# Performance work log

Measured on AMD Instinct MI355X. Metric: run time of the kernel, lower is better.

## Reference

```python
import jax, jax.numpy as jnp
import numpy as np

N_ATOMS = 4096
N_NEIGH = 32
IN_F = 128
HID = 256
OUT_F = 128
N_SPECIES = 64


def setup_inputs() -> dict:
    key = jax.random.key(0)
    k1, k2, k3, k4, k5, k6 = jax.random.split(key, 6)
    # kaiming-uniform-ish init scales (exact init doesn't matter for correctness testing)
    s1 = 1.0 / np.sqrt(IN_F)
    s2 = 1.0 / np.sqrt(HID)
    return {
        "features": jax.random.normal(k1, (N_ATOMS, N_NEIGH, IN_F), dtype=jnp.float32),
        "species_idx": jax.random.randint(k2, (N_ATOMS,), 0, N_SPECIES, dtype=jnp.int64 if jax.config.jax_enable_x64 else jnp.int32),
        "W1": jax.random.uniform(k3, (N_SPECIES, HID, IN_F), jnp.float32, -s1, s1),
        "b1": jax.random.uniform(k4, (N_SPECIES, HID), jnp.float32, -s1, s1),
        "W2": jax.random.uniform(k5, (N_SPECIES, OUT_F, HID), jnp.float32, -s2, s2),
        "b2": jax.random.uniform(k6, (N_SPECIES, OUT_F), jnp.float32, -s2, s2),
    }


def reference(features, species_idx, W1, b1, W2, b2):
    # Per-atom species-conditioned 2-layer MLP with SiLU after the hidden layer.
    # features: (A, N, in); W[idx]: (A, out, in) gathered per atom (as in torch W[idx]).
    x = jnp.einsum("ani,ahi->anh", features, W1[species_idx]) + b1[species_idx][:, None, :]
    x = jax.nn.silu(x)
    x = jnp.einsum("anh,aoh->ano", x, W2[species_idx]) + b2[species_idx][:, None, :]
    return x  # (A, N, out)
```

## Files before the change

kernel.cpp:

```cpp
#include <hip/hip_runtime.h>

typedef __attribute__((ext_vector_type(8))) short short8;
typedef __attribute__((ext_vector_type(4))) float f32x4;

#define N_ATOMS 4096
#define N_NEIGH 32
#define IN_F 128
#define HID 256
#define OUT_F 128
#define N_SPECIES 64
#define GRP 8
#define MAX_GROUPS 576

struct HL { short h, l; };
__device__ __forceinline__ HL split2(float v) {
  unsigned u = __float_as_uint(v);
  float lo = v - __uint_as_float(u & 0xFFFF0000u);
  HL o;
  o.h = (short)(u >> 16);
  o.l = (short)(__float_as_uint(lo) >> 16);
  return o;
}

__global__ __launch_bounds__(256) void prep_kernel(
    const float* __restrict__ W1, const float* __restrict__ W2,
    const int* __restrict__ sp_idx,
    unsigned short* __restrict__ w1h, unsigned short* __restrict__ w1l,
    unsigned short* __restrict__ w2h, unsigned short* __restrict__ w2l,
    int* __restrict__ atom_order, int* __restrict__ grp_sp,
    int* __restrict__ grp_base, int* __restrict__ grp_cnt,
    int* __restrict__ n_groups) {
  const int t = threadIdx.x;
  if (blockIdx.x == 0) {
    __shared__ int cnt[N_SPECIES], off[N_SPECIES], cur[N_SPECIES], gb[N_SPECIES];
    if (t < N_SPECIES) cnt[t] = 0;
    __syncthreads();
    for (int a = t; a < N_ATOMS; a += 256) atomicAdd(&cnt[sp_idx[a]], 1);
    __syncthreads();
    if (t == 0) {
      int o = 0, g = 0;
      for (int s = 0; s < N_SPECIES; ++s) {
        off[s] = o; cur[s] = o; gb[s] = g;
        o += cnt[s];
        g += (cnt[s] + GRP - 1) / GRP;
      }
      *n_groups = g;
    }
    __syncthreads();
    for (int a = t; a < N_ATOMS; a += 256) {
      int s = sp_idx[a];
      atom_order[atomicAdd(&cur[s], 1)] = a;
    }
    if (t < N_SPECIES) {
      const int c = cnt[t], base = off[t], g0 = gb[t];
      const int ng = (c + GRP - 1) / GRP;
      for (int j = 0; j < ng; ++j) {
        grp_sp[g0 + j]   = t;
        grp_base[g0 + j] = base + j * GRP;
        grp_cnt[g0 + j]  = min(GRP, c - j * GRP);
      }
    }
    return;
  }
  const int NV = (N_SPECIES * HID * IN_F) / 4;
  const int nsplit = (gridDim.x - 1) * 256;
  for (int v = (blockIdx.x - 1) * 256 + t; v < 2 * NV; v += nsplit) {
    const float4* src; unsigned short* dh; unsigned short* dl; int j;
    if (v < NV) { src = (const float4*)W1; dh = w1h; dl = w1l; j = v; }
    else        { src = (const float4*)W2; dh = w2h; dl = w2l; j = v - NV; }
    float4 f = src[j];
    float vv[4] = {f.x, f.y, f.z, f.w};
    ushort4 h, l;
    HL s0 = split2(vv[0]); h.x = (unsigned short)s0.h; l.x = (unsigned short)s0.l;
    HL s1 = split2(vv[1]); h.y = (unsigned short)s1.h; l.y = (unsigned short)s1.l;
    HL s2 = split2(vv[2]); h.z = (unsigned short)s2.h; l.z = (unsigned short)s2.l;
    HL s3 = split2(vv[3]); h.w = (unsigned short)s3.h; l.w = (unsigned short)s3.l;
    ((ushort4*)dh)[j] = h;
    ((ushort4*)dl)[j] = l;
  }
}

__global__ __launch_bounds__(512, 2) void mlp_kernel(
    const float* __restrict__ feat,
    const float* __restrict__ b1g, const float* __restrict__ b2g,
    const unsigned short* __restrict__ w1h, const unsigned short* __restrict__ w1l,
    const unsigned short* __restrict__ w2h, const unsigned short* __restrict__ w2l,
    const int* __restrict__ atom_order, const int* __restrict__ grp_sp,
    const int* __restrict__ grp_base, const int* __restrict__ grp_cnt,
    const int* __restrict__ n_groups,
    float* __restrict__ out) {
  const int bid = blockIdx.x;
  const int g = (bid & 7) * (MAX_GROUPS / 8) + (bid >> 3);
  if (g >= *n_groups) return;
  const int s = grp_sp[g];
  const int abase = grp_base[g];
  const int cnt = grp_cnt[g];
  const int tid = threadIdx.x;
  const int wave = tid >> 6, lane = tid & 63;
  const int q = lane >> 4, r = lane & 15;

  __shared__ short lw1[2][2][32 * IN_F];
  __shared__ short lw2[2][2][OUT_F * 32];
  __shared__ float lx[8][N_NEIGH * 32];

  const bool active = (wave < cnt);
  int atom = 0;

  const int plane = wave >> 1, half = wave & 1;
  const bool isw1 = (plane < 2);
  const unsigned short* pl = (plane == 0) ? w1h : (plane == 1) ? w1l
                           : (plane == 2) ? w2h : w2l;
  const char* gplane = (const char*)pl + (long)s * (HID * IN_F) * 2;
  const int hcstride = isw1 ? (32 * IN_F * 2) : (32 * 2);
  int srcoff[4], dstoff[4];
#pragma unroll
  for (int it = 0; it < 4; ++it) {
    const int b = half * 4096 + it * 1024 + lane * 16;
    if (isw1) {
      const int row = b >> 8;
      srcoff[it] = row * (IN_F * 2) + ((b & 255) ^ ((row & 7) << 4));
    } else {
      const int o = b >> 6;
      srcoff[it] = o * (HID * 2) + ((b & 63) ^ (((o >> 1) & 3) << 4));
    }
    dstoff[it] = b;
  }
  char* lplane0 = isw1 ? (char*)lw1[0][plane] : (char*)lw2[0][plane - 2];

  auto STAGE = [&](int buf, int hc) {
    const char* base = gplane + hc * hcstride;
    char* lp = lplane0 + buf * 16384;
#pragma unroll
    for (int it = 0; it < 4; ++it) {
      __builtin_amdgcn_global_load_lds(
          (const __attribute__((address_space(1))) unsigned int*)(base + srcoff[it]),
          (__attribute__((address_space(3))) unsigned int*)(lp + dstoff[it]),
          16, 0, 0);
    }
  };

  STAGE(0, 0);

  short8 fh[2][4], fl[2][4];
  if (active) {
    atom = atom_order[abase + wave];
    const float* fb = feat + (long)atom * (N_NEIGH * IN_F);
#pragma unroll
    for (int nt = 0; nt < 2; ++nt)
#pragma unroll
      for (int ks = 0; ks < 4; ++ks) {
        const float* p = fb + (16 * nt + r) * IN_F + 32 * ks + 8 * q;
        float4 v0 = *(const float4*)p;
        float4 v1 = *(const float4*)(p + 4);
        float vv[8] = {v0.x, v0.y, v0.z, v0.w, v1.x, v1.y, v1.z, v1.w};
        short8 h8, l8;
#pragma unroll
        for (int j = 0; j < 8; ++j) {
          HL hl = split2(vv[j]);
          h8[j] = hl.h;
          l8[j] = hl.l;
        }
        fh[nt][ks] = h8;
        fl[nt][ks] = l8;
      }
  }

  float b2v[8];
#pragma unroll
  for (int ot = 0; ot < 8; ++ot) b2v[ot] = b2g[s * OUT_F + 16 * ot + r];

  f32x4 oacc[2][8] = {};
  char* lxw = (char*)lx[wave];
  const int swz1 = (r & 7) << 4;
  const int swz2 = ((r >> 1) & 3) << 4;

  asm volatile("s_waitcnt vmcnt(0)" ::: "memory");
  __syncthreads();

  for (int hc = 0; hc < 8; ++hc) {
    const int buf = hc & 1;
    if (hc < 7) STAGE(buf ^ 1, hc + 1);

    if (active) {
      f32x4 xacc[2][2] = {};
      const char* L1h = (const char*)lw1[buf][0];
      const char* L1l = (const char*)lw1[buf][1];
#pragma unroll
      for (int ks = 0; ks < 4; ++ks) {
        const int koff = 64 * ks + 16 * q;
#pragma unroll
        for (int ht = 0; ht < 2; ++ht) {
          const int byte = (16 * ht + r) * 256 + (koff ^ swz1);
          short8 bh = *(const short8*)(L1h + byte);
          short8 bl = *(const short8*)(L1l + byte);
#pragma unroll
          for (int nt = 0; nt < 2; ++nt) {
            xacc[nt][ht] = __builtin_amdgcn_mfma_f32_16x16x32_bf16(fh[nt][ks], bh, xacc[nt][ht], 0, 0, 0);
            xacc[nt][ht] = __builtin_amdgcn_mfma_f32_16x16x32_bf16(fh[nt][ks], bl, xacc[nt][ht], 0, 0, 0);
            xacc[nt][ht] = __builtin_amdgcn_mfma_f32_16x16x32_bf16(fl[nt][ks], bh, xacc[nt][ht], 0, 0, 0);
          }
        }
      }
#pragma unroll
      for (int ht = 0; ht < 2; ++ht) {
        const float b1v = b1g[s * HID + hc * 32 + 16 * ht + r];
#pragma unroll
        for (int nt = 0; nt < 2; ++nt)
#pragma unroll
          for (int i = 0; i < 4; ++i) {
            const int n = 16 * nt + 4 * q + i;
            float v = xacc[nt][ht][i] + b1v;
            v = v * __builtin_amdgcn_rcpf(1.0f + __expf(-v));
            int byte = (n << 7) + ((r + 16 * ht) << 2);
            byte ^= (n & 7) << 4;
            *(float*)(lxw + byte) = v;
          }
      }
      short8 ah[2], al[2];
#pragma unroll
      for (int nt = 0; nt < 2; ++nt) {
        const int n = 16 * nt + r;
        const int base_b = (n << 7) + (q << 5);
        const int swz = (n & 7) << 4;
        float4 v0 = *(const float4*)(lxw + (base_b ^ swz));
        float4 v1 = *(const float4*)(lxw + ((base_b + 16) ^ swz));
        float vv[8] = {v0.x, v0.y, v0.z, v0.w, v1.x, v1.y, v1.z, v1.w};
        short8 h8, l8;
#pragma unroll
        for (int j = 0; j < 8; ++j) {
          HL hl = split2(vv[j]);
          h8[j] = hl.h;
          l8[j] = hl.l;
        }
        ah[nt] = h8;
        al[nt] = l8;
      }
      const char* L2h = (const char*)lw2[buf][0];
      const char* L2l = (const char*)lw2[buf][1];
#pragma unroll
      for (int ot = 0; ot < 8; ++ot) {
        const int byte = (16 * ot + r) * 64 + ((16 * q) ^ swz2);
        short8 bh = *(const short8*)(L2h + byte);
        short8 bl = *(const short8*)(L2l + byte);
#pragma unroll
        for (int nt = 0; nt < 2; ++nt) {
          oacc[nt][ot] = __builtin_amdgcn_mfma_f32_16x16x32_bf16(ah[nt], bh, oacc[nt][ot], 0, 0, 0);
          oacc[nt][ot] = __builtin_amdgcn_mfma_f32_16x16x32_bf16(ah[nt], bl, oacc[nt][ot], 0, 0, 0);
          oacc[nt][ot] = __builtin_amdgcn_mfma_f32_16x16x32_bf16(al[nt], bh, oacc[nt][ot], 0, 0, 0);
        }
      }
    }
    asm volatile("s_waitcnt vmcnt(0)" ::: "memory");
    __syncthreads();
  }

  if (active) {
    float* ob = out + (long)atom * (N_NEIGH * OUT_F);
#pragma unroll
    for (int nt = 0; nt < 2; ++nt)
#pragma unroll
      for (int ot = 0; ot < 8; ++ot)
#pragma unroll
        for (int i = 0; i < 4; ++i) {
          ob[(16 * nt + 4 * q + i) * OUT_F + 16 * ot + r] = oacc[nt][ot][i] + b2v[ot];
        }
  }
}

extern "C" void kernel_launch(void* const* d_in, const int* in_sizes, int n_in,
                              void* d_out, int out_size, void* d_ws, size_t ws_size,
                              hipStream_t stream) {
  const float* feat = (const float*)d_in[0];
  const int* sp     = (const int*)d_in[1];
  const float* W1   = (const float*)d_in[2];
  const float* b1   = (const float*)d_in[3];
  const float* W2   = (const float*)d_in[4];
  const float* b2   = (const float*)d_in[5];
  float* out = (float*)d_out;

  char* ws = (char*)d_ws;
  unsigned short* w1h = (unsigned short*)(ws + 0);
  unsigned short* w1l = (unsigned short*)(ws + 4194304);
  unsigned short* w2h = (unsigned short*)(ws + 8388608);
  unsigned short* w2l = (unsigned short*)(ws + 12582912);
  int* atom_order = (int*)(ws + 16777216);
  int* grp_sp     = (int*)(ws + 16777216 + 16384);
  int* grp_base   = (int*)(ws + 16777216 + 16384 + 4352);
  int* grp_cnt    = (int*)(ws + 16777216 + 16384 + 8704);
  int* n_groups   = (int*)(ws + 16777216 + 16384 + 13056);

  hipLaunchKernelGGL(prep_kernel, dim3(1025), dim3(256), 0, stream,
                     W1, W2, sp, w1h, w1l, w2h, w2l,
                     atom_order, grp_sp, grp_base, grp_cnt, n_groups);
  hipLaunchKernelGGL(mlp_kernel, dim3(MAX_GROUPS), dim3(512), 0, stream,
                     feat, b1, b2, w1h, w1l, w2h, w2l,
                     atom_order, grp_sp, grp_base, grp_cnt, n_groups, out);
}
```

Measured before the change: 205.7 us.

## Use single rounded bf16 weights and stage full species weights in LDS once

```diff
diff --git a/kernel.cpp b/kernel.cpp
--- a/kernel.cpp
+++ b/kernel.cpp
@@ -12,6 +12,11 @@
 #define GRP 8
 #define MAX_GROUPS 576
 
+__device__ __forceinline__ unsigned short f2bf(float f) {
+  unsigned u = __float_as_uint(f);
+  u += 0x7FFF + ((u >> 16) & 1);
+  return (unsigned short)(u >> 16);
+}
 struct HL { short h, l; };
 __device__ __forceinline__ HL split2(float v) {
   unsigned u = __float_as_uint(v);
@@ -25,8 +30,7 @@
 __global__ __launch_bounds__(256) void prep_kernel(
     const float* __restrict__ W1, const float* __restrict__ W2,
     const int* __restrict__ sp_idx,
-    unsigned short* __restrict__ w1h, unsigned short* __restrict__ w1l,
-    unsigned short* __restrict__ w2h, unsigned short* __restrict__ w2l,
+    unsigned short* __restrict__ w1h, unsigned short* __restrict__ w2h,
     int* __restrict__ atom_order, int* __restrict__ grp_sp,
     int* __restrict__ grp_base, int* __restrict__ grp_cnt,
     int* __restrict__ n_groups) {
@@ -65,30 +69,28 @@
   const int NV = (N_SPECIES * HID * IN_F) / 4;
   const int nsplit = (gridDim.x - 1) * 256;
   for (int v = (blockIdx.x - 1) * 256 + t; v < 2 * NV; v += nsplit) {
-    const float4* src; unsigned short* dh; unsigned short* dl; int j;
-    if (v < NV) { src = (const float4*)W1; dh = w1h; dl = w1l; j = v; }
-    else        { src = (const float4*)W2; dh = w2h; dl = w2l; j = v - NV; }
+    const float4* src; unsigned short* dh; int j;
+    if (v < NV) { src = (const float4*)W1; dh = w1h; j = v; }
+    else        { src = (const float4*)W2; dh = w2h; j = v - NV; }
     float4 f = src[j];
-    float vv[4] = {f.x, f.y, f.z, f.w};
-    ushort4 h, l;
-    HL s0 = split2(vv[0]); h.x = (unsigned short)s0.h; l.x = (unsigned short)s0.l;
-    HL s1 = split2(vv[1]); h.y = (unsigned short)s1.h; l.y = (unsigned short)s1.l;
-    HL s2 = split2(vv[2]); h.z = (unsigned short)s2.h; l.z = (unsigned short)s2.l;
-    HL s3 = split2(vv[3]); h.w = (unsigned short)s3.h; l.w = (unsigned short)s3.l;
+    ushort4 h;
+    h.x = f2bf(f.x); h.y = f2bf(f.y); h.z = f2bf(f.z); h.w = f2bf(f.w);
     ((ushort4*)dh)[j] = h;
-    ((ushort4*)dl)[j] = l;
   }
 }
 
 __global__ __launch_bounds__(512, 2) void mlp_kernel(
     const float* __restrict__ feat,
     const float* __restrict__ b1g, const float* __restrict__ b2g,
-    const unsigned short* __restrict__ w1h, const unsigned short* __restrict__ w1l,
-    const unsigned short* __restrict__ w2h, const unsigned short* __restrict__ w2l,
+    const unsigned short* __restrict__ w1h, const unsigned short* __restrict__ w2h,
     const int* __restrict__ atom_order, const int* __restrict__ grp_sp,
     const int* __restrict__ grp_base, const int* __restrict__ grp_cnt,
     const int* __restrict__ n_groups,
     float* __restrict__ out) {
+  extern __shared__ char smem[];
+  char* LW1 = smem;
+  char* LW2 = smem + 65536;
+
   const int bid = blockIdx.x;
   const int g = (bid & 7) * (MAX_GROUPS / 8) + (bid >> 3);
   if (g >= *n_groups) return;
@@ -98,50 +100,33 @@
   const int tid = threadIdx.x;
   const int wave = tid >> 6, lane = tid & 63;
   const int q = lane >> 4, r = lane & 15;
-
-  __shared__ short lw1[2][2][32 * IN_F];
-  __shared__ short lw2[2][2][OUT_F * 32];
-  __shared__ float lx[8][N_NEIGH * 32];
-
   const bool active = (wave < cnt);
+
+  {
+    const char* gw1 = (const char*)w1h + (long)s * (HID * IN_F * 2);
+    const char* gw2 = (const char*)w2h + (long)s * (OUT_F * HID * 2);
+#pragma unroll
+    for (int it = 0; it < 8; ++it) {
+      const int d = it * 8192 + tid * 16;
+      const int h = d >> 8, w = d & 255;
+      const int src = h * (IN_F * 2) + (w ^ ((h & 7) << 4));
+      __builtin_amdgcn_global_load_lds(
+          (const __attribute__((address_space(1))) unsigned int*)(gw1 + src),
+          (__attribute__((address_space(3))) unsigned int*)(LW1 + d), 16, 0, 0);
+    }
+#pragma unroll
+    for (int it = 0; it < 8; ++it) {
+      const int d = it * 8192 + tid * 16;
+      const int o = d >> 9, w = d & 511;
+      const int src = o * (HID * 2) + (w ^ ((o & 7) << 4));
+      __builtin_amdgcn_global_load_lds(
+          (const __attribute__((address_space(1))) unsigned int*)(gw2 + src),
+          (__attribute__((address_space(3))) unsigned int*)(LW2 + d), 16, 0, 0);
+    }
+  }
+
+  short8 fh[2][4], fl[2][4];
   int atom = 0;
-
-  const int plane = wave >> 1, half = wave & 1;
-  const bool isw1 = (plane < 2);
-  const unsigned short* pl = (plane == 0) ? w1h : (plane == 1) ? w1l
-                           : (plane == 2) ? w2h : w2l;
-  const char* gplane = (const char*)pl + (long)s * (HID * IN_F) * 2;
-  const int hcstride = isw1 ? (32 * IN_F * 2) : (32 * 2);
-  int srcoff[4], dstoff[4];
-#pragma unroll
-  for (int it = 0; it < 4; ++it) {
-    const int b = half * 4096 + it * 1024 + lane * 16;
-    if (isw1) {
-      const int row = b >> 8;
-      srcoff[it] = row * (IN_F * 2) + ((b & 255) ^ ((row & 7) << 4));
-    } else {
-      const int o = b >> 6;
-      srcoff[it] = o * (HID * 2) + ((b & 63) ^ (((o >> 1) & 3) << 4));
-    }
-    dstoff[it] = b;
-  }
-  char* lplane0 = isw1 ? (char*)lw1[0][plane] : (char*)lw2[0][plane - 2];
-
-  auto STAGE = [&](int buf, int hc) {
-    const char* base = gplane + hc * hcstride;
-    char* lp = lplane0 + buf * 16384;
-#pragma unroll
-    for (int it = 0; it < 4; ++it) {
-      __builtin_amdgcn_global_load_lds(
-          (const __attribute__((address_space(1))) unsigned int*)(base + srcoff[it]),
-          (__attribute__((address_space(3))) unsigned int*)(lp + dstoff[it]),
-          16, 0, 0);
-    }
-  };
-
-  STAGE(0, 0);
-
-  short8 fh[2][4], fl[2][4];
   if (active) {
     atom = atom_order[abase + wave];
     const float* fb = feat + (long)atom * (N_NEIGH * IN_F);
@@ -165,105 +150,85 @@
       }
   }
 
-  float b2v[8];
-#pragma unroll
-  for (int ot = 0; ot < 8; ++ot) b2v[ot] = b2g[s * OUT_F + 16 * ot + r];
-
-  f32x4 oacc[2][8] = {};
-  char* lxw = (char*)lx[wave];
-  const int swz1 = (r & 7) << 4;
-  const int swz2 = ((r >> 1) & 3) << 4;
-
   asm volatile("s_waitcnt vmcnt(0)" ::: "memory");
   __syncthreads();
 
+  if (!active) return;
+
+  f32x4 oacc[2][8] = {};
+  char* lxw = smem + 131072 + wave * 4096;
+  const int swz = (r & 7) << 4;
+  const float* b1s = b1g + s * HID;
+
   for (int hc = 0; hc < 8; ++hc) {
-    const int buf = hc & 1;
-    if (hc < 7) STAGE(buf ^ 1, hc + 1);
-
-    if (active) {
-      f32x4 xacc[2][2] = {};
-      const char* L1h = (const char*)lw1[buf][0];
-      const char* L1l = (const char*)lw1[buf][1];
-#pragma unroll
-      for (int ks = 0; ks < 4; ++ks) {
-        const int koff = 64 * ks + 16 * q;
-#pragma unroll
-        for (int ht = 0; ht < 2; ++ht) {
-          const int byte = (16 * ht + r) * 256 + (koff ^ swz1);
-          short8 bh = *(const short8*)(L1h + byte);
-          short8 bl = *(const short8*)(L1l + byte);
-#pragma unroll
-          for (int nt = 0; nt < 2; ++nt) {
-            xacc[nt][ht] = __builtin_amdgcn_mfma_f32_16x16x32_bf16(fh[nt][ks], bh, xacc[nt][ht], 0, 0, 0);
-            xacc[nt][ht] = __builtin_amdgcn_mfma_f32_16x16x32_bf16(fh[nt][ks], bl, xacc[nt][ht], 0, 0, 0);
-            xacc[nt][ht] = __builtin_amdgcn_mfma_f32_16x16x32_bf16(fl[nt][ks], bh, xacc[nt][ht], 0, 0, 0);
-          }
+    f32x4 xacc[2][2] = {};
+#pragma unroll
+    for (int ks = 0; ks < 4; ++ks) {
+      const int ib = ((32 * ks + 8 * q) * 2) ^ swz;
+#pragma unroll
+      for (int ht = 0; ht < 2; ++ht) {
+        const int row = 32 * hc + 16 * ht + r;
+        short8 bh = *(const short8*)(LW1 + row * 256 + ib);
+        xacc[0][ht] = __builtin_amdgcn_mfma_f32_16x16x32_bf16(fh[0][ks], bh, xacc[0][ht], 0, 0, 0);
+        xacc[1][ht] = __builtin_amdgcn_mfma_f32_16x16x32_bf16(fh[1][ks], bh, xacc[1][ht], 0, 0, 0);
+        xacc[0][ht] = __builtin_amdgcn_mfma_f32_16x16x32_bf16(fl[0][ks], bh, xacc[0][ht], 0, 0, 0);
+        xacc[1][ht] = __builtin_amdgcn_mfma_f32_16x16x32_bf16(fl[1][ks], bh, xacc[1][ht], 0, 0, 0);
+      }
+    }
+#pragma unroll
+    for (int ht = 0; ht < 2; ++ht) {
+      const float b1v = b1s[hc * 32 + 16 * ht + r];
+#pragma unroll
+      for (int nt = 0; nt < 2; ++nt)
+#pragma unroll
+        for (int i = 0; i < 4; ++i) {
+          const int n = 16 * nt + 4 * q + i;
+          float v = xacc[nt][ht][i] + b1v;
+          v = v * __builtin_amdgcn_rcpf(1.0f + __expf(-v));
+          const int byte = n * 128 + (((16 * ht + r) * 4) ^ ((q & 1) << 6));
+          *(float*)(lxw + byte) = v;
         }
-      }
-#pragma unroll
-      for (int ht = 0; ht < 2; ++ht) {
-        const float b1v = b1g[s * HID + hc * 32 + 16 * ht + r];
-#pragma unroll
-        for (int nt = 0; nt < 2; ++nt)
-#pragma unroll
-          for (int i = 0; i < 4; ++i) {
-            const int n = 16 * nt + 4 * q + i;
-            float v = xacc[nt][ht][i] + b1v;
-            v = v * __builtin_amdgcn_rcpf(1.0f + __expf(-v));
-            int byte = (n << 7) + ((r + 16 * ht) << 2);
-            byte ^= (n & 7) << 4;
-            *(float*)(lxw + byte) = v;
-          }
-      }
-      short8 ah[2], al[2];
-#pragma unroll
-      for (int nt = 0; nt < 2; ++nt) {
-        const int n = 16 * nt + r;
-        const int base_b = (n << 7) + (q << 5);
-        const int swz = (n & 7) << 4;
-        float4 v0 = *(const float4*)(lxw + (base_b ^ swz));
-        float4 v1 = *(const float4*)(lxw + ((base_b + 16) ^ swz));
-        float vv[8] = {v0.x, v0.y, v0.z, v0.w, v1.x, v1.y, v1.z, v1.w};
-        short8 h8, l8;
-#pragma unroll
-        for (int j = 0; j < 8; ++j) {
-          HL hl = split2(vv[j]);
-          h8[j] = hl.h;
-          l8[j] = hl.l;
-        }
-        ah[nt] = h8;
-        al[nt] = l8;
-      }
-      const char* L2h = (const char*)lw2[buf][0];
-      const char* L2l = (const char*)lw2[buf][1];
-#pragma unroll
-      for (int ot = 0; ot < 8; ++ot) {
-        const int byte = (16 * ot + r) * 64 + ((16 * q) ^ swz2);
-        short8 bh = *(const short8*)(L2h + byte);
-        short8 bl = *(const short8*)(L2l + byte);
-#pragma unroll
-        for (int nt = 0; nt < 2; ++nt) {
-          oacc[nt][ot] = __builtin_amdgcn_mfma_f32_16x16x32_bf16(ah[nt], bh, oacc[nt][ot], 0, 0, 0);
-          oacc[nt][ot] = __builtin_amdgcn_mfma_f32_16x16x32_bf16(ah[nt], bl, oacc[nt][ot], 0, 0, 0);
-          oacc[nt][ot] = __builtin_amdgcn_mfma_f32_16x16x32_bf16(al[nt], bh, oacc[nt][ot], 0, 0, 0);
-        }
-      }
-    }
-    asm volatile("s_waitcnt vmcnt(0)" ::: "memory");
-    __syncthreads();
-  }
-
-  if (active) {
-    float* ob = out + (long)atom * (N_NEIGH * OUT_F);
+    }
+    short8 ah[2], al[2];
+#pragma unroll
+    for (int nt = 0; nt < 2; ++nt) {
+      const int n = 16 * nt + r;
+      const int base_b = n * 128 + ((32 * q) ^ (((r >> 2) & 1) << 6));
+      float4 v0 = *(const float4*)(lxw + base_b);
+      float4 v1 = *(const float4*)(lxw + base_b + 16);
+      float vv[8] = {v0.x, v0.y, v0.z, v0.w, v1.x, v1.y, v1.z, v1.w};
+      short8 h8, l8;
+#pragma unroll
+      for (int j = 0; j < 8; ++j) {
+        HL hl = split2(vv[j]);
+        h8[j] = hl.h;
+        l8[j] = hl.l;
+      }
+      ah[nt] = h8;
+      al[nt] = l8;
+    }
+    const int kb = ((32 * hc + 8 * q) * 2) ^ swz;
+#pragma unroll
+    for (int ot = 0; ot < 8; ++ot) {
+      const int row = 16 * ot + r;
+      short8 bw = *(const short8*)(LW2 + row * 512 + kb);
+      oacc[0][ot] = __builtin_amdgcn_mfma_f32_16x16x32_bf16(ah[0], bw, oacc[0][ot], 0, 0, 0);
+      oacc[1][ot] = __builtin_amdgcn_mfma_f32_16x16x32_bf16(ah[1], bw, oacc[1][ot], 0, 0, 0);
+      oacc[0][ot] = __builtin_amdgcn_mfma_f32_16x16x32_bf16(al[0], bw, oacc[0][ot], 0, 0, 0);
+      oacc[1][ot] = __builtin_amdgcn_mfma_f32_16x16x32_bf16(al[1], bw, oacc[1][ot], 0, 0, 0);
+    }
+  }
+
+  float* ob = out + (long)atom * (N_NEIGH * OUT_F);
+#pragma unroll
+  for (int ot = 0; ot < 8; ++ot) {
+    const float b2v = b2g[s * OUT_F + 16 * ot + r];
 #pragma unroll
     for (int nt = 0; nt < 2; ++nt)
 #pragma unroll
-      for (int ot = 0; ot < 8; ++ot)
-#pragma unroll
-        for (int i = 0; i < 4; ++i) {
-          ob[(16 * nt + 4 * q + i) * OUT_F + 16 * ot + r] = oacc[nt][ot][i] + b2v[ot];
-        }
+      for (int i = 0; i < 4; ++i) {
+        ob[(16 * nt + 4 * q + i) * OUT_F + 16 * ot + r] = oacc[nt][ot][i] + b2v;
+      }
   }
 }
 
@@ -280,19 +245,20 @@
 
   char* ws = (char*)d_ws;
   unsigned short* w1h = (unsigned short*)(ws + 0);
-  unsigned short* w1l = (unsigned short*)(ws + 4194304);
-  unsigned short* w2h = (unsigned short*)(ws + 8388608);
-  unsigned short* w2l = (unsigned short*)(ws + 12582912);
-  int* atom_order = (int*)(ws + 16777216);
-  int* grp_sp     = (int*)(ws + 16777216 + 16384);
-  int* grp_base   = (int*)(ws + 16777216 + 16384 + 4352);
-  int* grp_cnt    = (int*)(ws + 16777216 + 16384 + 8704);
-  int* n_groups   = (int*)(ws + 16777216 + 16384 + 13056);
+  unsigned short* w2h = (unsigned short*)(ws + 4194304);
+  int* atom_order = (int*)(ws + 8388608);
+  int* grp_sp     = (int*)(ws + 8388608 + 16384);
+  int* grp_base   = (int*)(ws + 8388608 + 16384 + 4352);
+  int* grp_cnt    = (int*)(ws + 8388608 + 16384 + 8704);
+  int* n_groups   = (int*)(ws + 8388608 + 16384 + 13056);
+
+  hipFuncSetAttribute((const void*)mlp_kernel,
+                      hipFuncAttributeMaxDynamicSharedMemorySize, 163840);
 
   hipLaunchKernelGGL(prep_kernel, dim3(1025), dim3(256), 0, stream,
-                     W1, W2, sp, w1h, w1l, w2h, w2l,
+                     W1, W2, sp, w1h, w2h,
                      atom_order, grp_sp, grp_base, grp_cnt, n_groups);
-  hipLaunchKernelGGL(mlp_kernel, dim3(MAX_GROUPS), dim3(512), 0, stream,
-                     feat, b1, b2, w1h, w1l, w2h, w2l,
+  hipLaunchKernelGGL(mlp_kernel, dim3(MAX_GROUPS), dim3(512), 163840, stream,
+                     feat, b1, b2, w1h, w2h,
                      atom_order, grp_sp, grp_base, grp_cnt, n_groups, out);
 }
```

After: 192.2 us. 6.6% less time.
